# Performance work log

Hardware: AMD Instinct MI355X
Metric: run time of the kernel (lower is better)

## Reference

```python
import jax, jax.numpy as jnp
import numpy as np

N, E, G = 50000, 500000, 2048
HID, H, ED, L = 128, 4, 12, 8
D = HID // H
EPS_BN = 1e-5


def setup_inputs() -> dict:
    key = jax.random.key(0)
    ks = jax.random.split(key, 32)
    s = 0.05
    x = jax.random.normal(ks[0], (N, 22), jnp.float32)
    src = jax.random.randint(ks[1], (E,), 0, N)
    off = jax.random.randint(ks[2], (E,), 1, N)
    dst = (src + off) % N  # guaranteed no self-loops -> move_mask is all True
    batch = jnp.sort(jax.random.randint(ks[3], (N,), 0, G))
    edge_attr = jax.random.normal(ks[4], (E, ED), jnp.float32)
    params = dict(
        Win=jax.random.normal(ks[5], (22, HID), jnp.float32) * s,
        b_in=jnp.zeros((HID,), jnp.float32),
        Wl=jax.random.normal(ks[6], (L, HID, HID), jnp.float32) * s,
        bl=jnp.zeros((L, HID), jnp.float32),
        Wr=jax.random.normal(ks[7], (L, HID, HID), jnp.float32) * s,
        br=jnp.zeros((L, HID), jnp.float32),
        We=jax.random.normal(ks[8], (L, ED, HID), jnp.float32) * s,
        att=jax.random.normal(ks[9], (L, H, D), jnp.float32) * s,
        bo=jnp.zeros((L, HID), jnp.float32),
        gamma=jnp.ones((L, HID), jnp.float32),
        beta=jnp.zeros((L, HID), jnp.float32),
        Wv1=jax.random.normal(ks[10], (HID, 64), jnp.float32) * s,
        bv1=jnp.zeros((64,), jnp.float32),
        Wv2=jax.random.normal(ks[11], (64, 3), jnp.float32) * s,
        bv2=jnp.zeros((3,), jnp.float32),
        Wp1=jax.random.normal(ks[12], (2 * HID + ED, 64), jnp.float32) * s,
        bp1=jnp.zeros((64,), jnp.float32),
        Wp2=jax.random.normal(ks[13], (64, 1), jnp.float32) * s,
        bp2=jnp.zeros((1,), jnp.float32),
    )
    return dict(x=x, src=src, dst=dst, batch=batch, edge_attr=edge_attr, **params)


def _bn(h, g, b):
    mu = h.mean(0)
    var = h.var(0)
    return (h - mu) * jax.lax.rsqrt(var + EPS_BN) * g + b


def _gatv2(h, src, dst, edge_attr, Wl, bl, Wr, br, We, att, bo):
    xl = (h @ Wl + bl).reshape(N, H, D)   # source-side (values + score)
    xr = (h @ Wr + br).reshape(N, H, D)   # target-side (score)
    e = (edge_attr @ We).reshape(E, H, D)
    sc = xl[src] + xr[dst] + e            # [E,H,D]
    sc = jnp.where(sc > 0, sc, 0.2 * sc)  # LeakyReLU(0.2)
    a = jnp.einsum('ehd,hd->eh', sc, att)  # [E,H]
    m = jax.ops.segment_max(a, dst, num_segments=N)
    ex = jnp.exp(a - m[dst])
    den = jax.ops.segment_sum(ex, dst, num_segments=N)
    alpha = ex / (den[dst] + 1e-16)        # per-destination softmax
    out = jax.ops.segment_sum(xl[src] * alpha[..., None], dst, num_segments=N)
    return out.reshape(N, HID) + bo


def reference(x, src, dst, batch, edge_attr, Win, b_in, Wl, bl, Wr, br, We, att,
              bo, gamma, beta, Wv1, bv1, Wv2, bv2, Wp1, bp1, Wp2, bp2):
    h = jax.nn.relu(x @ Win + b_in)
    for blk in range(L // 2):
        i, j = 2 * blk, 2 * blk + 1
        res = h
        h = jax.nn.relu(_bn(_gatv2(h, src, dst, edge_attr, Wl[i], bl[i], Wr[i], br[i], We[i], att[i], bo[i]), gamma[i], beta[i]))
        h = _bn(_gatv2(h, src, dst, edge_attr, Wl[j], bl[j], Wr[j], br[j], We[j], att[j], bo[j]), gamma[j], beta[j])
        h = jax.nn.relu(h + res)
    cnt = jax.ops.segment_sum(jnp.ones((N,), h.dtype), batch, num_segments=G)
    pooled = jax.ops.segment_sum(h, batch, num_segments=G) / jnp.maximum(cnt, 1.0)[:, None]
    value_logits = jax.nn.relu(pooled @ Wv1 + bv1) @ Wv2 + bv2   # [G,3]
    edge_in = jnp.concatenate([h[src], h[dst], edge_attr], axis=1)  # [E, 2*HID+ED]
    policy_logits = (jax.nn.relu(edge_in @ Wp1 + bp1) @ Wp2 + bp2)[:, 0]  # [E]
    return (value_logits, policy_logits)
```

## Files before the change

kernel.cpp:

```cpp
#include <hip/hip_runtime.h>
#include <math.h>

#define N_NODES 50000
#define N_EDGES 500000
#define N_GRAPHS 2048
#define HID 128
#define EDIM 12
#define NLAYERS 8
#define EPS_BN 1e-5f
#define LOG2E 1.44269504088896340736f
#define GAT_BLOCKS 2048
#define GAT_WAVES (GAT_BLOCKS * 4)

typedef __attribute__((ext_vector_type(8))) short short8;
typedef __attribute__((ext_vector_type(4))) float f32x4;
typedef __attribute__((ext_vector_type(2))) float f32x2;
typedef unsigned int uint;
typedef unsigned short ushort;

__device__ inline ushort f2bf(float x) {
  unsigned u = __float_as_uint(x);
  u = (u + 0x7FFFu + ((u >> 16) & 1u)) >> 16;
  return (ushort)u;
}
__device__ inline unsigned pk_bf16(float a, float b) {
  return (unsigned)f2bf(a) | ((unsigned)f2bf(b) << 16);
}
__device__ inline float bflo(uint q) { return __uint_as_float(q << 16); }
__device__ inline float bfhi(uint q) { return __uint_as_float(q & 0xFFFF0000u); }
__device__ inline f32x2 pfma(f32x2 a, f32x2 b, f32x2 c) {
  return __builtin_elementwise_fma(a, b, c);
}
template <int CTRL>
__device__ inline float dpp_add(float v) {
  int s = __builtin_amdgcn_update_dpp(0, __float_as_int(v), CTRL, 0xF, 0xF, true);
  return v + __int_as_float(s);
}
#define RED8(v)               \
  v = dpp_add<0xB1>(v);       \
  v = dpp_add<0x4E>(v);       \
  v = dpp_add<0x141>(v);

__global__ void zero_kernel(int* deg, int* cursor, float* stats, uint* erec) {
  int i = blockIdx.x * 256 + threadIdx.x;
  if (i < N_NODES) { deg[i] = 0; cursor[i] = 0; }
  if (i < NLAYERS * 256) stats[i] = 0.f;
  if (i < 32) erec[(size_t)N_EDGES * 8 + i] = 0u;
}

__global__ void count_kernel(const int* __restrict__ dst, int* __restrict__ deg) {
  int e = blockIdx.x * 256 + threadIdx.x;
  if (e < N_EDGES) atomicAdd(&deg[dst[e]], 1);
}

__global__ void scan1_kernel(int* __restrict__ off, int* __restrict__ bsum) {
  __shared__ int s[256];
  int t = threadIdx.x; int n = blockIdx.x * 256 + t;
  int x = (n < N_NODES) ? off[n] : 0;
  s[t] = x; __syncthreads();
  for (int o = 1; o < 256; o <<= 1) {
    int v = (t >= o) ? s[t - o] : 0;
    __syncthreads(); s[t] += v; __syncthreads();
  }
  if (n < N_NODES) off[n] = s[t] - x;
  if (t == 255) bsum[blockIdx.x] = s[255];
}

__global__ void scan2_kernel(int* __restrict__ bsum, int nb) {
  __shared__ int s[256];
  int t = threadIdx.x;
  int x = (t < nb) ? bsum[t] : 0;
  s[t] = x; __syncthreads();
  for (int o = 1; o < 256; o <<= 1) {
    int v = (t >= o) ? s[t - o] : 0;
    __syncthreads(); s[t] += v; __syncthreads();
  }
  if (t < nb) bsum[t] = s[t] - x;
}

__global__ void scan3_kernel(int* __restrict__ off, const int* __restrict__ bsum) {
  int t = threadIdx.x; int n = blockIdx.x * 256 + t;
  if (n < N_NODES) off[n] += bsum[blockIdx.x];
  if (n == 0 && blockIdx.x == 0) off[N_NODES] = N_EDGES;
}

__global__ void scatter_kernel(const int* __restrict__ src, const int* __restrict__ dst,
                               const float* __restrict__ ea,
                               const int* __restrict__ off, int* __restrict__ cursor,
                               uint* __restrict__ erec) {
  int e = blockIdx.x * 256 + threadIdx.x;
  if (e < N_EDGES) {
    int d = dst[e];
    int p = atomicAdd(&cursor[d], 1);
    int pos = off[d] + p;
    const float* eap = &ea[(size_t)e * EDIM];
    float4 e0 = *(const float4*)eap;
    float4 e1 = *(const float4*)(eap + 4);
    float4 e2 = *(const float4*)(eap + 8);
    uint4 q0, q1;
    q0.x = (uint)src[e]; q0.y = 0u;
    q0.z = pk_bf16(e0.x, e0.y); q0.w = pk_bf16(e0.z, e0.w);
    q1.x = pk_bf16(e1.x, e1.y); q1.y = pk_bf16(e1.z, e1.w);
    q1.z = pk_bf16(e2.x, e2.y); q1.w = pk_bf16(e2.z, e2.w);
    uint* o = &erec[(size_t)pos * 8];
    *(uint4*)o = q0;
    *(uint4*)(o + 4) = q1;
  }
}

__global__ void wprep_kernel(const float* __restrict__ Wl, const float* __restrict__ Wr,
                             ushort* __restrict__ wpk) {
  int idx = blockIdx.x * 256 + threadIdx.x;
  if (idx >= NLAYERS * 4 * 256 * 32) return;
  int kk = idx & 31;
  int cc = (idx >> 5) & 255;
  int kb = (idx >> 13) & 3;
  int layer = idx >> 15;
  int k = kb * 32 + kk;
  float v = (cc < 128) ? Wl[((size_t)layer * 128 + k) * 128 + cc]
                       : Wr[((size_t)layer * 128 + k) * 128 + (cc - 128)];
  wpk[idx] = f2bf(v);
}

__global__ void wprep_pol_kernel(const float* __restrict__ Wp1, ushort* __restrict__ wppk) {
  int idx = blockIdx.x * 256 + threadIdx.x;
  if (idx >= 4 * 128 * 32) return;
  int kk = idx & 31;
  int cc = (idx >> 5) & 127;
  int kb = idx >> 12;
  int k = kb * 32 + kk;
  float v = (cc < 64) ? Wp1[(size_t)k * 64 + cc] : Wp1[(size_t)(128 + k) * 64 + (cc - 64)];
  wppk[idx] = f2bf(v);
}

__global__ void inproj_kernel(const float* __restrict__ x, const float* __restrict__ Win,
                              const float* __restrict__ b_in, float* __restrict__ h,
                              ushort* __restrict__ h16) {
  __shared__ float xs[44];
  int t = threadIdx.x;
  int n0 = blockIdx.x * 2;
  if (t < 44) xs[t] = x[n0 * 22 + t];
  __syncthreads();
  int c = t & 127, half = t >> 7;
  int n = n0 + half;
  if (n < N_NODES) {
    float acc = b_in[c];
#pragma unroll
    for (int k = 0; k < 22; k++) acc = fmaf(xs[half * 22 + k], Win[k * HID + c], acc);
    float v = fmaxf(acc, 0.f);
    h[(size_t)n * HID + c] = v;
    h16[(size_t)n * HID + c] = f2bf(v);
  }
}

template <int NOUT, int SPLIT, bool BIAS, bool OUTBF16, bool BNFUSE, bool RESID, bool WRITEH>
__global__ __launch_bounds__(256) void gemm_mfma_kernel(
    const ushort* __restrict__ A16, const ushort* __restrict__ T16,
    const float* __restrict__ stats, const float* __restrict__ gamma,
    const float* __restrict__ beta, const float* __restrict__ res,
    float* __restrict__ hout,
    const ushort* __restrict__ Wpk, const float* __restrict__ b1,
    const float* __restrict__ b2, void* __restrict__ C1v, void* __restrict__ C2v,
    int nrows) {
  __shared__ ushort As[64][136];
  int t = threadIdx.x;
  int brow = blockIdx.x * 64;
  if constexpr (!BNFUSE) {
#pragma unroll
    for (int i = 0; i < 4; i++) {
      int f = t + i * 256;
      int r = f >> 4, cg = (f & 15) * 8;
      int g = brow + r;
      uint4 v = make_uint4(0, 0, 0, 0);
      if (g < nrows) v = *(const uint4*)&A16[(size_t)g * HID + cg];
      *(uint4*)&As[r][cg] = v;
    }
  } else {
    int cg = (t & 31) * 4;
    int r0 = t >> 5;
    const float invN = 1.f / (float)N_NODES;
    float4 sm = *(const float4*)&stats[cg];
    float4 sq = *(const float4*)&stats[128 + cg];
    float4 gm = *(const float4*)&gamma[cg];
    float4 bt = *(const float4*)&beta[cg];
    float s4[4] = {sm.x, sm.y, sm.z, sm.w};
    float q4[4] = {sq.x, sq.y, sq.z, sq.w};
    float g4[4] = {gm.x, gm.y, gm.z, gm.w};
    float bb4[4] = {bt.x, bt.y, bt.z, bt.w};
    float scl[4], shf[4];
#pragma unroll
    for (int k = 0; k < 4; k++) {
      float mu = s4[k] * invN;
      float var = q4[k] * invN - mu * mu;
      float rs = rsqrtf(var + EPS_BN);
      scl[k] = g4[k] * rs;
      shf[k] = bb4[k] - mu * scl[k];
    }
#pragma unroll
    for (int rr = 0; rr < 8; rr++) {
      int r = r0 + rr * 8;
      int g = brow + r;
      uint2 tvu = make_uint2(0u, 0u);
      if (g < nrows) tvu = *(const uint2*)&T16[(size_t)g * HID + cg];
      float o0 = fmaf(bflo(tvu.x), scl[0], shf[0]);
      float o1 = fmaf(bfhi(tvu.x), scl[1], shf[1]);
      float o2 = fmaf(bflo(tvu.y), scl[2], shf[2]);
      float o3 = fmaf(bfhi(tvu.y), scl[3], shf[3]);
      if constexpr (RESID) {
        if (g < nrows) {
          float4 rv = *(const float4*)&res[(size_t)g * HID + cg];
          o0 += rv.x; o1 += rv.y; o2 += rv.z; o3 += rv.w;
        }
      }
      o0 = fmaxf(o0, 0.f); o1 = fmaxf(o1, 0.f);
      o2 = fmaxf(o2, 0.f); o3 = fmaxf(o3, 0.f);
      if constexpr (WRITEH) {
        if (g < nrows) {
          float4 ov = make_float4(o0, o1, o2, o3);
          *(float4*)&hout[(size_t)g * HID + cg] = ov;
        }
      }
      *(uint2*)&As[r][cg] = make_uint2(pk_bf16(o0, o1), pk_bf16(o2, o3));
    }
  }
  __syncthreads();
  int lane = t & 63, wave = t >> 6;
  int arow = wave * 16 + (lane & 15);
  int k8 = (lane >> 4) * 8;
  constexpr int NT = NOUT / 16;
  f32x4 acc[NT];
#pragma unroll
  for (int n = 0; n < NT; n++) acc[n] = (f32x4){0.f, 0.f, 0.f, 0.f};
#pragma unroll
  for (int kb = 0; kb < 4; kb++) {
    short8 a = *(const short8*)&As[arow][kb * 32 + k8];
#pragma unroll
    for (int n = 0; n < NT; n++) {
      int col = n * 16 + (lane & 15);
      short8 b = *(const short8*)&Wpk[((size_t)(kb * NOUT + col)) * 32 + k8];
      acc[n] = __builtin_amdgcn_mfma_f32_16x16x32_bf16(a, b, acc[n], 0, 0, 0);
    }
  }
  int rbase = brow + wave * 16 + (lane >> 4) * 4;
  int ccol = lane & 15;
#pragma unroll
  for (int n = 0; n < NT; n++) {
    int col = n * 16 + ccol;
    float bias = 0.f;
    if (BIAS) bias = (col < SPLIT) ? b1[col] : b2[col - SPLIT];
    int colw = (col < SPLIT) ? col : col - SPLIT;
#pragma unroll
    for (int j = 0; j < 4; j++) {
      int row = rbase + j;
      if (row < nrows) {
        float v = acc[n][j] + bias;
        if (OUTBF16) {
          ushort* dstp = (ushort*)((col < SPLIT) ? C1v : C2v);
          dstp[(size_t)row * SPLIT + colw] = f2bf(v);
        } else {
          float* dstp = (float*)((col < SPLIT) ? C1v : C2v);
          dstp[(size_t)row * SPLIT + colw] = v;
        }
      }
    }
  }
}

#define GAT_EDGE4(ra, rb, xw, OKEXPR)                                        \
  {                                                                          \
    f32x2 xa01 = (f32x2){bflo(xw.x), bfhi(xw.x)};                            \
    f32x2 xa23 = (f32x2){bflo(xw.y), bfhi(xw.y)};                            \
    f32x2 ep01 = xa01 + xr01;                                                \
    f32x2 ep23 = xa23 + xr23;                                                \
    uint q; float lo, hi;                                                    \
    q = ra.z; lo = bflo(q); hi = bfhi(q);                                    \
    ep01 = pfma((f32x2){lo, lo}, wk01[0], ep01);                             \
    ep23 = pfma((f32x2){lo, lo}, wk23[0], ep23);                             \
    ep01 = pfma((f32x2){hi, hi}, wk01[1], ep01);                             \
    ep23 = pfma((f32x2){hi, hi}, wk23[1], ep23);                             \
    q = ra.w; lo = bflo(q); hi = bfhi(q);                                    \
    ep01 = pfma((f32x2){lo, lo}, wk01[2], ep01);                             \
    ep23 = pfma((f32x2){lo, lo}, wk23[2], ep23);                             \
    ep01 = pfma((f32x2){hi, hi}, wk01[3], ep01);                             \
    ep23 = pfma((f32x2){hi, hi}, wk23[3], ep23);                             \
    q = rb.x; lo = bflo(q); hi = bfhi(q);                                    \
    ep01 = pfma((f32x2){lo, lo}, wk01[4], ep01);                             \
    ep23 = pfma((f32x2){lo, lo}, wk23[4], ep23);                             \
    ep01 = pfma((f32x2){hi, hi}, wk01[5], ep01);                             \
    ep23 = pfma((f32x2){hi, hi}, wk23[5], ep23);                             \
    q = rb.y; lo = bflo(q); hi = bfhi(q);                                    \
    ep01 = pfma((f32x2){lo, lo}, wk01[6], ep01);                             \
    ep23 = pfma((f32x2){lo, lo}, wk23[6], ep23);                             \
    ep01 = pfma((f32x2){hi, hi}, wk01[7], ep01);                             \
    ep23 = pfma((f32x2){hi, hi}, wk23[7], ep23);                             \
    q = rb.z; lo = bflo(q); hi = bfhi(q);                                    \
    ep01 = pfma((f32x2){lo, lo}, wk01[8], ep01);                             \
    ep23 = pfma((f32x2){lo, lo}, wk23[8], ep23);                             \
    ep01 = pfma((f32x2){hi, hi}, wk01[9], ep01);                             \
    ep23 = pfma((f32x2){hi, hi}, wk23[9], ep23);                             \
    q = rb.w; lo = bflo(q); hi = bfhi(q);                                    \
    ep01 = pfma((f32x2){lo, lo}, wk01[10], ep01);                            \
    ep23 = pfma((f32x2){lo, lo}, wk23[10], ep23);                            \
    ep01 = pfma((f32x2){hi, hi}, wk01[11], ep01);                            \
    ep23 = pfma((f32x2){hi, hi}, wk23[11], ep23);                            \
    f32x2 s01 = __builtin_elementwise_max(ep01, ep01 * (f32x2){0.2f, 0.2f}); \
    f32x2 s23 = __builtin_elementwise_max(ep23, ep23 * (f32x2){0.2f, 0.2f}); \
    float v = fmaf(s01.x, at4.x,                                             \
              fmaf(s01.y, at4.y, fmaf(s23.x, at4.z, s23.y * at4.w)));        \
    RED8(v)                                                                  \
    bool ok = (OKEXPR);                                                      \
    float dm = v - m;                                                        \
    float e = __builtin_amdgcn_exp2f(-fabsf(dm));                            \
    bool big = dm > 0.f;                                                     \
    float sc = (big && ok) ? e : 1.f;                                        \
    float p = ok ? (big ? 1.f : e) : 0.f;                                    \
    m = (ok && big) ? v : m;                                                 \
    d = fmaf(d, sc, p);                                                      \
    acc01 = pfma(acc01, (f32x2){sc, sc}, (f32x2){p, p} * xa01);              \
    acc23 = pfma(acc23, (f32x2){sc, sc}, (f32x2){p, p} * xa23);              \
  }

__global__ __launch_bounds__(256) void gat_kernel(
    const ushort* __restrict__ xl16, const ushort* __restrict__ xr16,
    const uint* __restrict__ erec, const int* __restrict__ off,
    const float* __restrict__ Wel, const float* __restrict__ attl,
    const float* __restrict__ bol, ushort* __restrict__ out16) {
  int lane = threadIdx.x & 63;
  int gwave = blockIdx.x * 4 + (threadIdx.x >> 6);
  int half = lane >> 5;
  int c0 = (lane & 31) * 4;

  f32x2 wk01[12], wk23[12];
#pragma unroll
  for (int k = 0; k < 12; k++) {
    float4 w = *(const float4*)&Wel[k * HID + c0];
    wk01[k] = (f32x2){w.x, w.y};
    wk23[k] = (f32x2){w.z, w.w};
  }
  float4 at4 = *(const float4*)&attl[c0];
  at4.x *= LOG2E; at4.y *= LOG2E; at4.z *= LOG2E; at4.w *= LOG2E;
  float4 bo = *(const float4*)&bol[c0];

  for (int node = gwave; node < N_NODES; node += GAT_WAVES) {
    uint2 xru = *(const uint2*)&xr16[((uint)node << 7) + c0];
    f32x2 xr01 = (f32x2){bflo(xru.x), bfhi(xru.x)};
    f32x2 xr23 = (f32x2){bflo(xru.y), bfhi(xru.y)};

    int is = off[node], deg = off[node + 1] - is;

    float m = -INFINITY, d = 0.f;
    f32x2 acc01 = (f32x2){0.f, 0.f};
    f32x2 acc23 = (f32x2){0.f, 0.f};

    if (deg > 0) {
      const uint* pe = erec + ((size_t)is + half) * 8;
      uint4 Ra = *(const uint4*)pe, Rb = *(const uint4*)(pe + 4);
      uint2 xw = *(const uint2*)&xl16[(Ra.x << 7) + c0];
      int full = deg >> 1;
      for (int i = 0; i < full; i++) {
        const uint* pn = pe + 16;
        uint4 Na = *(const uint4*)pn, Nb = *(const uint4*)(pn + 4);
        uint2 xn = *(const uint2*)&xl16[(Na.x << 7) + c0];
        GAT_EDGE4(Ra, Rb, xw, true)
        Ra = Na; Rb = Nb; xw = xn; pe = pn;
      }
      if (deg & 1) GAT_EDGE4(Ra, Rb, xw, half == 0)
    }

    float mo = __shfl_xor(m, 32);
    float dd = __shfl_xor(d, 32);
    f32x2 o01, o23;
    o01.x = __shfl_xor(acc01.x, 32); o01.y = __shfl_xor(acc01.y, 32);
    o23.x = __shfl_xor(acc23.x, 32); o23.y = __shfl_xor(acc23.y, 32);
    float mn = fmaxf(m, mo);
    float wS = (m > -INFINITY) ? __builtin_amdgcn_exp2f(m - mn) : 0.f;
    float wO = (mo > -INFINITY) ? __builtin_amdgcn_exp2f(mo - mn) : 0.f;
    float den = d * wS + dd * wO;
    f32x2 a01 = acc01 * (f32x2){wS, wS} + o01 * (f32x2){wO, wO};
    f32x2 a23 = acc23 * (f32x2){wS, wS} + o23 * (f32x2){wO, wO};
    float inv = 1.f / (den + 1e-16f);
    if (half == 0) {
      uint2 o;
      o.x = pk_bf16(fmaf(a01.x, inv, bo.x), fmaf(a01.y, inv, bo.y));
      o.y = pk_bf16(fmaf(a23.x, inv, bo.z), fmaf(a23.y, inv, bo.w));
      *(uint2*)&out16[((uint)node << 7) + c0] = o;
    }
  }
}

__global__ void bnstats_kernel(const ushort* __restrict__ t16, float* __restrict__ sums) {
  int tid = threadIdx.x;
  int c2 = (tid & 63) * 2;
  int grp = tid >> 6;
  float s0 = 0.f, s1 = 0.f, q0 = 0.f, q1 = 0.f;
  for (int n = blockIdx.x * 4 + grp; n < N_NODES; n += 1024) {
    uint v = *(const uint*)&t16[((uint)n << 7) + c2];
    float a = bflo(v), b = bfhi(v);
    s0 += a; q0 = fmaf(a, a, q0);
    s1 += b; q1 = fmaf(b, b, q1);
  }
  __shared__ float ls[4][128], lq[4][128];
  *(float2*)&ls[grp][c2] = make_float2(s0, s1);
  *(float2*)&lq[grp][c2] = make_float2(q0, q1);
  __syncthreads();
  if (tid < 128) {
    float s = ls[0][tid] + ls[1][tid] + ls[2][tid] + ls[3][tid];
    atomicAdd(&sums[tid], s);
    float q = lq[0][tid] + lq[1][tid] + lq[2][tid] + lq[3][tid];
    atomicAdd(&sums[128 + tid], q);
  }
}

__global__ __launch_bounds__(256) void policy_kernel(
    const ushort* __restrict__ Ps, const ushort* __restrict__ Pd,
    const int* __restrict__ src, const int* __restrict__ dst,
    const float* __restrict__ edge_attr, const float* __restrict__ Wp1e,
    const float* __restrict__ bp1, const float* __restrict__ Wp2,
    const float* __restrict__ bp2, float* __restrict__ outp) {
  int j = threadIdx.x & 15;
  int gid = (blockIdx.x * 256 + threadIdx.x) >> 4;
  int ngroups = (gridDim.x * 256) >> 4;
  float4 we[12];
#pragma unroll
  for (int k = 0; k < 12; k++) we[k] = *(const float4*)&Wp1e[k * 64 + j * 4];
  float4 b4 = *(const float4*)&bp1[j * 4];
  float4 w2 = *(const float4*)&Wp2[j * 4];
  float bp2c = bp2[0];
  for (int e = gid; e < N_EDGES; e += ngroups) {
    int s = src[e], d = dst[e];
    const float* eap = &edge_attr[(size_t)e * EDIM];
    float4 e0 = *(const float4*)eap;
    float4 e1 = *(const float4*)(eap + 4);
    float4 e2 = *(const float4*)(eap + 8);
    uint2 psu = *(const uint2*)&Ps[(size_t)s * 64 + j * 4];
    uint2 pdu = *(const uint2*)&Pd[(size_t)d * 64 + j * 4];
    float eav[12] = {e0.x, e0.y, e0.z, e0.w, e1.x, e1.y, e1.z, e1.w, e2.x, e2.y, e2.z, e2.w};
    float hx = bflo(psu.x) + bflo(pdu.x) + b4.x;
    float hy = bfhi(psu.x) + bfhi(pdu.x) + b4.y;
    float hz = bflo(psu.y) + bflo(pdu.y) + b4.z;
    float hw = bfhi(psu.y) + bfhi(pdu.y) + b4.w;
#pragma unroll
    for (int k = 0; k < 12; k++) {
      hx = fmaf(eav[k], we[k].x, hx);
      hy = fmaf(eav[k], we[k].y, hy);
      hz = fmaf(eav[k], we[k].z, hz);
      hw = fmaf(eav[k], we[k].w, hw);
    }
    hx = fmaxf(hx, 0.f); hy = fmaxf(hy, 0.f); hz = fmaxf(hz, 0.f); hw = fmaxf(hw, 0.f);
    float v = fmaf(hx, w2.x, fmaf(hy, w2.y, fmaf(hz, w2.z, hw * w2.w)));
    v += __shfl_xor(v, 1);
    v += __shfl_xor(v, 2);
    v += __shfl_xor(v, 4);
    v += __shfl_xor(v, 8);
    if (j == 0) outp[e] = v + bp2c;
  }
}

__device__ int lower_bound_dev(const int* a, int n, int key) {
  int lo = 0, hi = n;
  while (lo < hi) {
    int mid = (lo + hi) >> 1;
    if (a[mid] < key) lo = mid + 1; else hi = mid;
  }
  return lo;
}

__global__ void poolvalue_kernel(const float* __restrict__ h, const int* __restrict__ batch,
                                 const float* __restrict__ Wv1, const float* __restrict__ bv1,
                                 const float* __restrict__ Wv2, const float* __restrict__ bv2,
                                 float* __restrict__ outv) {
  __shared__ float pl[128];
  __shared__ float hd[64];
  __shared__ int range[2];
  int g = blockIdx.x, t = threadIdx.x;
  if (t == 0) {
    range[0] = lower_bound_dev(batch, N_NODES, g);
    range[1] = lower_bound_dev(batch, N_NODES, g + 1);
  }
  __syncthreads();
  int lo = range[0], hi = range[1];
  float s = 0.f;
  for (int n = lo; n < hi; n++) s += h[(size_t)n * HID + t];
  float cnt = (float)(hi - lo);
  pl[t] = s / fmaxf(cnt, 1.f);
  __syncthreads();
  if (t < 64) {
    float a = bv1[t];
    for (int c = 0; c < 128; c++) a = fmaf(pl[c], Wv1[c * 64 + t], a);
    hd[t] = fmaxf(a, 0.f);
  }
  __syncthreads();
  if (t < 3) {
    float a = bv2[t];
    for (int j = 0; j < 64; j++) a = fmaf(hd[j], Wv2[j * 3 + t], a);
    outv[g * 3 + t] = a;
  }
}

extern "C" void kernel_launch(void* const* d_in, const int* in_sizes, int n_in,
                              void* d_out, int out_size, void* d_ws, size_t ws_size,
                              hipStream_t stream) {
  (void)in_sizes; (void)n_in; (void)out_size; (void)ws_size;
  const float* x    = (const float*)d_in[0];
  const int*   src  = (const int*)d_in[1];
  const int*   dst  = (const int*)d_in[2];
  const int*   batch= (const int*)d_in[3];
  const float* ea   = (const float*)d_in[4];
  const float* Win  = (const float*)d_in[5];
  const float* b_in = (const float*)d_in[6];
  const float* Wl   = (const float*)d_in[7];
  const float* bl   = (const float*)d_in[8];
  const float* Wr   = (const float*)d_in[9];
  const float* br   = (const float*)d_in[10];
  const float* We   = (const float*)d_in[11];
  const float* att  = (const float*)d_in[12];
  const float* bo   = (const float*)d_in[13];
  const float* gamma= (const float*)d_in[14];
  const float* beta = (const float*)d_in[15];
  const float* Wv1  = (const float*)d_in[16];
  const float* bv1  = (const float*)d_in[17];
  const float* Wv2  = (const float*)d_in[18];
  const float* bv2  = (const float*)d_in[19];
  const float* Wp1  = (const float*)d_in[20];
  const float* bp1  = (const float*)d_in[21];
  const float* Wp2  = (const float*)d_in[22];
  const float* bp2  = (const float*)d_in[23];

  float* outv = (float*)d_out;
  float* outp = outv + (size_t)N_GRAPHS * 3;

  float* hres   = (float*)d_ws;
  ushort* tmp16 = (ushort*)(hres + (size_t)N_NODES * HID);
  ushort* h16   = tmp16 + (size_t)N_NODES * HID;
  ushort* xl16  = h16 + (size_t)N_NODES * HID;
  ushort* xr16  = xl16 + (size_t)N_NODES * HID;
  float* stats  = (float*)(xr16 + (size_t)N_NODES * HID);
  ushort* wpk   = (ushort*)(stats + NLAYERS * 256);
  ushort* wppk  = wpk + (size_t)NLAYERS * 4 * 256 * 32;
  int* off    = (int*)(wppk + 4 * 128 * 32);
  int* cursor = off + (N_NODES + 1);
  int* bsum   = cursor + N_NODES;
  uint* erec  = (uint*)(((uintptr_t)(bsum + 256) + 15) & ~(uintptr_t)15);

  const int NB = (N_NODES + 255) / 256;
  const int EB = (N_EDGES + 255) / 256;

  zero_kernel<<<NB, 256, 0, stream>>>(off, cursor, stats, erec);
  count_kernel<<<EB, 256, 0, stream>>>(dst, off);
  scan1_kernel<<<NB, 256, 0, stream>>>(off, bsum);
  scan2_kernel<<<1, 256, 0, stream>>>(bsum, NB);
  scan3_kernel<<<NB, 256, 0, stream>>>(off, bsum);
  scatter_kernel<<<EB, 256, 0, stream>>>(src, dst, ea, off, cursor, erec);
  wprep_kernel<<<(NLAYERS * 4 * 256 * 32 + 255) / 256, 256, 0, stream>>>(Wl, Wr, wpk);
  wprep_pol_kernel<<<(4 * 128 * 32 + 255) / 256, 256, 0, stream>>>(Wp1, wppk);
  inproj_kernel<<<N_NODES / 2, 256, 0, stream>>>(x, Win, b_in, hres, h16);

  const int MB = (N_NODES + 63) / 64;

  for (int l = 0; l < NLAYERS; l++) {
    if (l == 0) {
      gemm_mfma_kernel<256, 128, true, true, false, false, false><<<MB, 256, 0, stream>>>(
          h16, nullptr, nullptr, nullptr, nullptr, nullptr, nullptr,
          wpk, bl, br, xl16, xr16, N_NODES);
    } else if (l & 1) {
      int p = l - 1;
      gemm_mfma_kernel<256, 128, true, true, true, false, false><<<MB, 256, 0, stream>>>(
          nullptr, tmp16, stats + p * 256, gamma + p * HID, beta + p * HID, nullptr, nullptr,
          wpk + (size_t)l * 32768, bl + l * HID, br + l * HID, xl16, xr16, N_NODES);
    } else {
      int p = l - 1;
      gemm_mfma_kernel<256, 128, true, true, true, true, true><<<MB, 256, 0, stream>>>(
          nullptr, tmp16, stats + p * 256, gamma + p * HID, beta + p * HID, hres, hres,
          wpk + (size_t)l * 32768, bl + l * HID, br + l * HID, xl16, xr16, N_NODES);
    }
    gat_kernel<<<GAT_BLOCKS, 256, 0, stream>>>(xl16, xr16, erec, off,
                                               We + (size_t)l * EDIM * HID, att + (size_t)l * HID,
                                               bo + (size_t)l * HID, tmp16);
    bnstats_kernel<<<256, 256, 0, stream>>>(tmp16, stats + l * 256);
  }

  ushort* Ps = xl16;
  ushort* Pd = xr16;
  gemm_mfma_kernel<128, 64, false, true, true, true, true><<<MB, 256, 0, stream>>>(
      nullptr, tmp16, stats + 7 * 256, gamma + 7 * HID, beta + 7 * HID, hres, hres,
      wppk, nullptr, nullptr, Ps, Pd, N_NODES);
  policy_kernel<<<2048, 256, 0, stream>>>(Ps, Pd, src, dst, ea,
                                          Wp1 + 256 * 64, bp1, Wp2, bp2, outp);
  poolvalue_kernel<<<N_GRAPHS, 128, 0, stream>>>(hres, batch, Wv1, bv1, Wv2, bv2, outv);
}
```

Measured before the change: 1.153 ms.

## Fuse BN stats into GAT kernel, merge prep and head kernels, fp32 intermediates

```diff
diff --git a/kernel.cpp b/kernel.cpp
--- a/kernel.cpp
+++ b/kernel.cpp
@@ -40,13 +40,6 @@
   v = dpp_add<0xB1>(v);       \
   v = dpp_add<0x4E>(v);       \
   v = dpp_add<0x141>(v);
-
-__global__ void zero_kernel(int* deg, int* cursor, float* stats, uint* erec) {
-  int i = blockIdx.x * 256 + threadIdx.x;
-  if (i < N_NODES) { deg[i] = 0; cursor[i] = 0; }
-  if (i < NLAYERS * 256) stats[i] = 0.f;
-  if (i < 32) erec[(size_t)N_EDGES * 8 + i] = 0u;
-}
 
 __global__ void count_kernel(const int* __restrict__ dst, int* __restrict__ deg) {
   int e = blockIdx.x * 256 + threadIdx.x;
@@ -108,29 +101,33 @@
   }
 }
 
-__global__ void wprep_kernel(const float* __restrict__ Wl, const float* __restrict__ Wr,
-                             ushort* __restrict__ wpk) {
-  int idx = blockIdx.x * 256 + threadIdx.x;
-  if (idx >= NLAYERS * 4 * 256 * 32) return;
-  int kk = idx & 31;
-  int cc = (idx >> 5) & 255;
-  int kb = (idx >> 13) & 3;
-  int layer = idx >> 15;
-  int k = kb * 32 + kk;
-  float v = (cc < 128) ? Wl[((size_t)layer * 128 + k) * 128 + cc]
-                       : Wr[((size_t)layer * 128 + k) * 128 + (cc - 128)];
-  wpk[idx] = f2bf(v);
-}
-
-__global__ void wprep_pol_kernel(const float* __restrict__ Wp1, ushort* __restrict__ wppk) {
-  int idx = blockIdx.x * 256 + threadIdx.x;
-  if (idx >= 4 * 128 * 32) return;
-  int kk = idx & 31;
-  int cc = (idx >> 5) & 127;
-  int kb = idx >> 12;
-  int k = kb * 32 + kk;
-  float v = (cc < 64) ? Wp1[(size_t)k * 64 + cc] : Wp1[(size_t)(128 + k) * 64 + (cc - 64)];
-  wppk[idx] = f2bf(v);
+__global__ void prep_kernel(int* __restrict__ off, int* __restrict__ cursor,
+                            float* __restrict__ stats, uint* __restrict__ erec,
+                            const float* __restrict__ Wl, const float* __restrict__ Wr,
+                            ushort* __restrict__ wpk,
+                            const float* __restrict__ Wp1, ushort* __restrict__ wppk) {
+  int i = blockIdx.x * 256 + threadIdx.x;
+  if (i < N_NODES) { off[i] = 0; cursor[i] = 0; }
+  if (i < NLAYERS * 8 * 256) stats[i] = 0.f;
+  if (i < 32) erec[(size_t)N_EDGES * 8 + i] = 0u;
+  if (i < NLAYERS * 4 * 256 * 32) {
+    int kk = i & 31;
+    int cc = (i >> 5) & 255;
+    int kb = (i >> 13) & 3;
+    int layer = i >> 15;
+    int k = kb * 32 + kk;
+    float v = (cc < 128) ? Wl[((size_t)layer * 128 + k) * 128 + cc]
+                         : Wr[((size_t)layer * 128 + k) * 128 + (cc - 128)];
+    wpk[i] = f2bf(v);
+  }
+  if (i < 4 * 128 * 32) {
+    int kk = i & 31;
+    int cc = (i >> 5) & 127;
+    int kb = i >> 12;
+    int k = kb * 32 + kk;
+    float v = (cc < 64) ? Wp1[(size_t)k * 64 + cc] : Wp1[(size_t)(128 + k) * 64 + (cc - 64)];
+    wppk[i] = f2bf(v);
+  }
 }
 
 __global__ void inproj_kernel(const float* __restrict__ x, const float* __restrict__ Win,
@@ -155,8 +152,8 @@
 
 template <int NOUT, int SPLIT, bool BIAS, bool OUTBF16, bool BNFUSE, bool RESID, bool WRITEH>
 __global__ __launch_bounds__(256) void gemm_mfma_kernel(
-    const ushort* __restrict__ A16, const ushort* __restrict__ T16,
-    const float* __restrict__ stats, const float* __restrict__ gamma,
+    const ushort* __restrict__ A16, const float* __restrict__ T,
+    const float* __restrict__ stats8, const float* __restrict__ gamma,
     const float* __restrict__ beta, const float* __restrict__ res,
     float* __restrict__ hout,
     const ushort* __restrict__ Wpk, const float* __restrict__ b1,
@@ -179,12 +176,17 @@
     int cg = (t & 31) * 4;
     int r0 = t >> 5;
     const float invN = 1.f / (float)N_NODES;
-    float4 sm = *(const float4*)&stats[cg];
-    float4 sq = *(const float4*)&stats[128 + cg];
+    float s4[4] = {0.f, 0.f, 0.f, 0.f};
+    float q4[4] = {0.f, 0.f, 0.f, 0.f};
+#pragma unroll
+    for (int sl = 0; sl < 8; sl++) {
+      float4 a = *(const float4*)&stats8[sl * 256 + cg];
+      float4 b = *(const float4*)&stats8[sl * 256 + 128 + cg];
+      s4[0] += a.x; s4[1] += a.y; s4[2] += a.z; s4[3] += a.w;
+      q4[0] += b.x; q4[1] += b.y; q4[2] += b.z; q4[3] += b.w;
+    }
     float4 gm = *(const float4*)&gamma[cg];
     float4 bt = *(const float4*)&beta[cg];
-    float s4[4] = {sm.x, sm.y, sm.z, sm.w};
-    float q4[4] = {sq.x, sq.y, sq.z, sq.w};
     float g4[4] = {gm.x, gm.y, gm.z, gm.w};
     float bb4[4] = {bt.x, bt.y, bt.z, bt.w};
     float scl[4], shf[4];
@@ -200,12 +202,12 @@
     for (int rr = 0; rr < 8; rr++) {
       int r = r0 + rr * 8;
       int g = brow + r;
-      uint2 tvu = make_uint2(0u, 0u);
-      if (g < nrows) tvu = *(const uint2*)&T16[(size_t)g * HID + cg];
-      float o0 = fmaf(bflo(tvu.x), scl[0], shf[0]);
-      float o1 = fmaf(bfhi(tvu.x), scl[1], shf[1]);
-      float o2 = fmaf(bflo(tvu.y), scl[2], shf[2]);
-      float o3 = fmaf(bfhi(tvu.y), scl[3], shf[3]);
+      float4 tv = make_float4(0.f, 0.f, 0.f, 0.f);
+      if (g < nrows) tv = *(const float4*)&T[(size_t)g * HID + cg];
+      float o0 = fmaf(tv.x, scl[0], shf[0]);
+      float o1 = fmaf(tv.y, scl[1], shf[1]);
+      float o2 = fmaf(tv.z, scl[2], shf[2]);
+      float o3 = fmaf(tv.w, scl[3], shf[3]);
       if constexpr (RESID) {
         if (g < nrows) {
           float4 rv = *(const float4*)&res[(size_t)g * HID + cg];
@@ -324,7 +326,8 @@
     const ushort* __restrict__ xl16, const ushort* __restrict__ xr16,
     const uint* __restrict__ erec, const int* __restrict__ off,
     const float* __restrict__ Wel, const float* __restrict__ attl,
-    const float* __restrict__ bol, ushort* __restrict__ out16) {
+    const float* __restrict__ bol, float* __restrict__ out,
+    float* __restrict__ stats) {
   int lane = threadIdx.x & 63;
   int gwave = blockIdx.x * 4 + (threadIdx.x >> 6);
   int half = lane >> 5;
@@ -340,6 +343,9 @@
   float4 at4 = *(const float4*)&attl[c0];
   at4.x *= LOG2E; at4.y *= LOG2E; at4.z *= LOG2E; at4.w *= LOG2E;
   float4 bo = *(const float4*)&bol[c0];
+
+  float ps0 = 0.f, ps1 = 0.f, ps2 = 0.f, ps3 = 0.f;
+  float pq0 = 0.f, pq1 = 0.f, pq2 = 0.f, pq3 = 0.f;
 
   for (int node = gwave; node < N_NODES; node += GAT_WAVES) {
     uint2 xru = *(const uint2*)&xr16[((uint)node << 7) + c0];
@@ -380,79 +386,34 @@
     f32x2 a23 = acc23 * (f32x2){wS, wS} + o23 * (f32x2){wO, wO};
     float inv = 1.f / (den + 1e-16f);
     if (half == 0) {
-      uint2 o;
-      o.x = pk_bf16(fmaf(a01.x, inv, bo.x), fmaf(a01.y, inv, bo.y));
-      o.y = pk_bf16(fmaf(a23.x, inv, bo.z), fmaf(a23.y, inv, bo.w));
-      *(uint2*)&out16[((uint)node << 7) + c0] = o;
-    }
-  }
-}
-
-__global__ void bnstats_kernel(const ushort* __restrict__ t16, float* __restrict__ sums) {
-  int tid = threadIdx.x;
-  int c2 = (tid & 63) * 2;
-  int grp = tid >> 6;
-  float s0 = 0.f, s1 = 0.f, q0 = 0.f, q1 = 0.f;
-  for (int n = blockIdx.x * 4 + grp; n < N_NODES; n += 1024) {
-    uint v = *(const uint*)&t16[((uint)n << 7) + c2];
-    float a = bflo(v), b = bfhi(v);
-    s0 += a; q0 = fmaf(a, a, q0);
-    s1 += b; q1 = fmaf(b, b, q1);
-  }
+      float r0 = fmaf(a01.x, inv, bo.x);
+      float r1 = fmaf(a01.y, inv, bo.y);
+      float r2 = fmaf(a23.x, inv, bo.z);
+      float r3 = fmaf(a23.y, inv, bo.w);
+      *(float4*)&out[((uint)node << 7) + c0] = make_float4(r0, r1, r2, r3);
+      ps0 += r0; pq0 = fmaf(r0, r0, pq0);
+      ps1 += r1; pq1 = fmaf(r1, r1, pq1);
+      ps2 += r2; pq2 = fmaf(r2, r2, pq2);
+      ps3 += r3; pq3 = fmaf(r3, r3, pq3);
+    }
+  }
+
   __shared__ float ls[4][128], lq[4][128];
-  *(float2*)&ls[grp][c2] = make_float2(s0, s1);
-  *(float2*)&lq[grp][c2] = make_float2(q0, q1);
+  int wv = threadIdx.x >> 6;
+  if (half == 0) {
+    ls[wv][c0 + 0] = ps0; ls[wv][c0 + 1] = ps1;
+    ls[wv][c0 + 2] = ps2; ls[wv][c0 + 3] = ps3;
+    lq[wv][c0 + 0] = pq0; lq[wv][c0 + 1] = pq1;
+    lq[wv][c0 + 2] = pq2; lq[wv][c0 + 3] = pq3;
+  }
   __syncthreads();
-  if (tid < 128) {
-    float s = ls[0][tid] + ls[1][tid] + ls[2][tid] + ls[3][tid];
-    atomicAdd(&sums[tid], s);
-    float q = lq[0][tid] + lq[1][tid] + lq[2][tid] + lq[3][tid];
-    atomicAdd(&sums[128 + tid], q);
-  }
-}
-
-__global__ __launch_bounds__(256) void policy_kernel(
-    const ushort* __restrict__ Ps, const ushort* __restrict__ Pd,
-    const int* __restrict__ src, const int* __restrict__ dst,
-    const float* __restrict__ edge_attr, const float* __restrict__ Wp1e,
-    const float* __restrict__ bp1, const float* __restrict__ Wp2,
-    const float* __restrict__ bp2, float* __restrict__ outp) {
-  int j = threadIdx.x & 15;
-  int gid = (blockIdx.x * 256 + threadIdx.x) >> 4;
-  int ngroups = (gridDim.x * 256) >> 4;
-  float4 we[12];
-#pragma unroll
-  for (int k = 0; k < 12; k++) we[k] = *(const float4*)&Wp1e[k * 64 + j * 4];
-  float4 b4 = *(const float4*)&bp1[j * 4];
-  float4 w2 = *(const float4*)&Wp2[j * 4];
-  float bp2c = bp2[0];
-  for (int e = gid; e < N_EDGES; e += ngroups) {
-    int s = src[e], d = dst[e];
-    const float* eap = &edge_attr[(size_t)e * EDIM];
-    float4 e0 = *(const float4*)eap;
-    float4 e1 = *(const float4*)(eap + 4);
-    float4 e2 = *(const float4*)(eap + 8);
-    uint2 psu = *(const uint2*)&Ps[(size_t)s * 64 + j * 4];
-    uint2 pdu = *(const uint2*)&Pd[(size_t)d * 64 + j * 4];
-    float eav[12] = {e0.x, e0.y, e0.z, e0.w, e1.x, e1.y, e1.z, e1.w, e2.x, e2.y, e2.z, e2.w};
-    float hx = bflo(psu.x) + bflo(pdu.x) + b4.x;
-    float hy = bfhi(psu.x) + bfhi(pdu.x) + b4.y;
-    float hz = bflo(psu.y) + bflo(pdu.y) + b4.z;
-    float hw = bfhi(psu.y) + bfhi(pdu.y) + b4.w;
-#pragma unroll
-    for (int k = 0; k < 12; k++) {
-      hx = fmaf(eav[k], we[k].x, hx);
-      hy = fmaf(eav[k], we[k].y, hy);
-      hz = fmaf(eav[k], we[k].z, hz);
-      hw = fmaf(eav[k], we[k].w, hw);
-    }
-    hx = fmaxf(hx, 0.f); hy = fmaxf(hy, 0.f); hz = fmaxf(hz, 0.f); hw = fmaxf(hw, 0.f);
-    float v = fmaf(hx, w2.x, fmaf(hy, w2.y, fmaf(hz, w2.z, hw * w2.w)));
-    v += __shfl_xor(v, 1);
-    v += __shfl_xor(v, 2);
-    v += __shfl_xor(v, 4);
-    v += __shfl_xor(v, 8);
-    if (j == 0) outp[e] = v + bp2c;
+  int t = threadIdx.x;
+  float* slice = stats + (blockIdx.x & 7) * 256;
+  if (t < 128) {
+    atomicAdd(&slice[t], ls[0][t] + ls[1][t] + ls[2][t] + ls[3][t]);
+  } else if (t < 256) {
+    int c = t - 128;
+    atomicAdd(&slice[128 + c], lq[0][c] + lq[1][c] + lq[2][c] + lq[3][c]);
   }
 }
 
@@ -465,35 +426,83 @@
   return lo;
 }
 
-__global__ void poolvalue_kernel(const float* __restrict__ h, const int* __restrict__ batch,
-                                 const float* __restrict__ Wv1, const float* __restrict__ bv1,
-                                 const float* __restrict__ Wv2, const float* __restrict__ bv2,
-                                 float* __restrict__ outv) {
-  __shared__ float pl[128];
-  __shared__ float hd[64];
-  __shared__ int range[2];
-  int g = blockIdx.x, t = threadIdx.x;
-  if (t == 0) {
-    range[0] = lower_bound_dev(batch, N_NODES, g);
-    range[1] = lower_bound_dev(batch, N_NODES, g + 1);
-  }
-  __syncthreads();
-  int lo = range[0], hi = range[1];
-  float s = 0.f;
-  for (int n = lo; n < hi; n++) s += h[(size_t)n * HID + t];
-  float cnt = (float)(hi - lo);
-  pl[t] = s / fmaxf(cnt, 1.f);
-  __syncthreads();
-  if (t < 64) {
-    float a = bv1[t];
-    for (int c = 0; c < 128; c++) a = fmaf(pl[c], Wv1[c * 64 + t], a);
-    hd[t] = fmaxf(a, 0.f);
-  }
-  __syncthreads();
-  if (t < 3) {
-    float a = bv2[t];
-    for (int j = 0; j < 64; j++) a = fmaf(hd[j], Wv2[j * 3 + t], a);
-    outv[g * 3 + t] = a;
+__global__ __launch_bounds__(256) void heads_kernel(
+    const float* __restrict__ Ps, const float* __restrict__ Pd,
+    const int* __restrict__ src, const int* __restrict__ dst,
+    const float* __restrict__ edge_attr, const float* __restrict__ Wp1e,
+    const float* __restrict__ bp1, const float* __restrict__ Wp2,
+    const float* __restrict__ bp2, float* __restrict__ outp,
+    const float* __restrict__ h, const int* __restrict__ batch,
+    const float* __restrict__ Wv1, const float* __restrict__ bv1,
+    const float* __restrict__ Wv2, const float* __restrict__ bv2,
+    float* __restrict__ outv) {
+  if (blockIdx.x < 2048) {
+    int j = threadIdx.x & 15;
+    int gid = (blockIdx.x * 256 + threadIdx.x) >> 4;
+    const int ngroups = (2048 * 256) >> 4;
+    float4 we[12];
+#pragma unroll
+    for (int k = 0; k < 12; k++) we[k] = *(const float4*)&Wp1e[k * 64 + j * 4];
+    float4 b4 = *(const float4*)&bp1[j * 4];
+    float4 w2 = *(const float4*)&Wp2[j * 4];
+    float bp2c = bp2[0];
+    for (int e = gid; e < N_EDGES; e += ngroups) {
+      int s = src[e], d = dst[e];
+      const float* eap = &edge_attr[(size_t)e * EDIM];
+      float4 e0 = *(const float4*)eap;
+      float4 e1 = *(const float4*)(eap + 4);
+      float4 e2 = *(const float4*)(eap + 8);
+      float4 psv = *(const float4*)&Ps[(size_t)s * 64 + j * 4];
+      float4 pdv = *(const float4*)&Pd[(size_t)d * 64 + j * 4];
+      float eav[12] = {e0.x, e0.y, e0.z, e0.w, e1.x, e1.y, e1.z, e1.w, e2.x, e2.y, e2.z, e2.w};
+      float hx = psv.x + pdv.x + b4.x;
+      float hy = psv.y + pdv.y + b4.y;
+      float hz = psv.z + pdv.z + b4.z;
+      float hw = psv.w + pdv.w + b4.w;
+#pragma unroll
+      for (int k = 0; k < 12; k++) {
+        hx = fmaf(eav[k], we[k].x, hx);
+        hy = fmaf(eav[k], we[k].y, hy);
+        hz = fmaf(eav[k], we[k].z, hz);
+        hw = fmaf(eav[k], we[k].w, hw);
+      }
+      hx = fmaxf(hx, 0.f); hy = fmaxf(hy, 0.f); hz = fmaxf(hz, 0.f); hw = fmaxf(hw, 0.f);
+      float v = fmaf(hx, w2.x, fmaf(hy, w2.y, fmaf(hz, w2.z, hw * w2.w)));
+      v += __shfl_xor(v, 1);
+      v += __shfl_xor(v, 2);
+      v += __shfl_xor(v, 4);
+      v += __shfl_xor(v, 8);
+      if (j == 0) outp[e] = v + bp2c;
+    }
+  } else {
+    __shared__ float pl[128];
+    __shared__ float hd[64];
+    __shared__ int range[2];
+    int g = blockIdx.x - 2048, t = threadIdx.x;
+    if (t == 0) {
+      range[0] = lower_bound_dev(batch, N_NODES, g);
+      range[1] = lower_bound_dev(batch, N_NODES, g + 1);
+    }
+    __syncthreads();
+    int lo = range[0], hi = range[1];
+    if (t < 128) {
+      float s = 0.f;
+      for (int n = lo; n < hi; n++) s += h[(size_t)n * HID + t];
+      float cnt = (float)(hi - lo);
+      pl[t] = s / fmaxf(cnt, 1.f);
+    }
+    __syncthreads();
+    if (t < 64) {
+      float a = bv1[t];
+      for (int c = 0; c < 128; c++) a = fmaf(pl[c], Wv1[c * 64 + t], a);
+      hd[t] = fmaxf(a, 0.f);
+    }
+    __syncthreads();
+    if (t < 3) {
+      float a = bv2[t];
+      for (int j = 0; j < 64; j++) a = fmaf(hd[j], Wv2[j * 3 + t], a);
+      outv[g * 3 + t] = a;
+    }
   }
 }
 
@@ -530,12 +539,12 @@
   float* outp = outv + (size_t)N_GRAPHS * 3;
 
   float* hres   = (float*)d_ws;
-  ushort* tmp16 = (ushort*)(hres + (size_t)N_NODES * HID);
-  ushort* h16   = tmp16 + (size_t)N_NODES * HID;
+  float* tmp    = hres + (size_t)N_NODES * HID;
+  ushort* h16   = (ushort*)(tmp + (size_t)N_NODES * HID);
   ushort* xl16  = h16 + (size_t)N_NODES * HID;
   ushort* xr16  = xl16 + (size_t)N_NODES * HID;
   float* stats  = (float*)(xr16 + (size_t)N_NODES * HID);
-  ushort* wpk   = (ushort*)(stats + NLAYERS * 256);
+  ushort* wpk   = (ushort*)(stats + NLAYERS * 8 * 256);
   ushort* wppk  = wpk + (size_t)NLAYERS * 4 * 256 * 32;
   int* off    = (int*)(wppk + 4 * 128 * 32);
   int* cursor = off + (N_NODES + 1);
@@ -544,15 +553,14 @@
 
   const int NB = (N_NODES + 255) / 256;
   const int EB = (N_EDGES + 255) / 256;
-
-  zero_kernel<<<NB, 256, 0, stream>>>(off, cursor, stats, erec);
+  const int PB = (NLAYERS * 4 * 256 * 32 + 255) / 256;
+
+  prep_kernel<<<PB, 256, 0, stream>>>(off, cursor, stats, erec, Wl, Wr, wpk, Wp1, wppk);
   count_kernel<<<EB, 256, 0, stream>>>(dst, off);
   scan1_kernel<<<NB, 256, 0, stream>>>(off, bsum);
   scan2_kernel<<<1, 256, 0, stream>>>(bsum, NB);
   scan3_kernel<<<NB, 256, 0, stream>>>(off, bsum);
   scatter_kernel<<<EB, 256, 0, stream>>>(src, dst, ea, off, cursor, erec);
-  wprep_kernel<<<(NLAYERS * 4 * 256 * 32 + 255) / 256, 256, 0, stream>>>(Wl, Wr, wpk);
-  wprep_pol_kernel<<<(4 * 128 * 32 + 255) / 256, 256, 0, stream>>>(Wp1, wppk);
   inproj_kernel<<<N_NODES / 2, 256, 0, stream>>>(x, Win, b_in, hres, h16);
 
   const int MB = (N_NODES + 63) / 64;
@@ -565,26 +573,25 @@
     } else if (l & 1) {
       int p = l - 1;
       gemm_mfma_kernel<256, 128, true, true, true, false, false><<<MB, 256, 0, stream>>>(
-          nullptr, tmp16, stats + p * 256, gamma + p * HID, beta + p * HID, nullptr, nullptr,
+          nullptr, tmp, stats + p * 2048, gamma + p * HID, beta + p * HID, nullptr, nullptr,
           wpk + (size_t)l * 32768, bl + l * HID, br + l * HID, xl16, xr16, N_NODES);
     } else {
       int p = l - 1;
       gemm_mfma_kernel<256, 128, true, true, true, true, true><<<MB, 256, 0, stream>>>(
-          nullptr, tmp16, stats + p * 256, gamma + p * HID, beta + p * HID, hres, hres,
+          nullptr, tmp, stats + p * 2048, gamma + p * HID, beta + p * HID, hres, hres,
           wpk + (size_t)l * 32768, bl + l * HID, br + l * HID, xl16, xr16, N_NODES);
     }
     gat_kernel<<<GAT_BLOCKS, 256, 0, stream>>>(xl16, xr16, erec, off,
                                                We + (size_t)l * EDIM * HID, att + (size_t)l * HID,
-                                               bo + (size_t)l * HID, tmp16);
-    bnstats_kernel<<<256, 256, 0, stream>>>(tmp16, stats + l * 256);
-  }
-
-  ushort* Ps = xl16;
-  ushort* Pd = xr16;
-  gemm_mfma_kernel<128, 64, false, true, true, true, true><<<MB, 256, 0, stream>>>(
-      nullptr, tmp16, stats + 7 * 256, gamma + 7 * HID, beta + 7 * HID, hres, hres,
+                                               bo + (size_t)l * HID, tmp, stats + l * 2048);
+  }
+
+  float* Ps = (float*)xl16;
+  float* Pd = (float*)xr16;
+  gemm_mfma_kernel<128, 64, false, false, true, true, true><<<MB, 256, 0, stream>>>(
+      nullptr, tmp, stats + 7 * 2048, gamma + 7 * HID, beta + 7 * HID, hres, hres,
       wppk, nullptr, nullptr, Ps, Pd, N_NODES);
-  policy_kernel<<<2048, 256, 0, stream>>>(Ps, Pd, src, dst, ea,
-                                          Wp1 + 256 * 64, bp1, Wp2, bp2, outp);
-  poolvalue_kernel<<<N_GRAPHS, 128, 0, stream>>>(hres, batch, Wv1, bv1, Wv2, bv2, outv);
-}
+  heads_kernel<<<4096, 256, 0, stream>>>(Ps, Pd, src, dst, ea,
+                                         Wp1 + 256 * 64, bp1, Wp2, bp2, outp,
+                                         hres, batch, Wv1, bv1, Wv2, bv2, outv);
+}
```

After: 1.096 ms (median of 2 runs). 1.05x faster.
